# Optimization experiments

Hardware: AMD Instinct MI355X
Metric: run time of the kernel (lower is better)

## Reference

```python
import jax, jax.numpy as jnp
import numpy as np

N_FFT = 1024
HOP = 256
WIN_LENGTH = 1024
B = 16
T = 480000


def setup_inputs() -> dict:
    key = jax.random.key(0)
    k1, k2 = jax.random.split(key)
    x = jax.random.normal(k1, (B, T), dtype=jnp.float32)
    window = jax.random.uniform(k2, (WIN_LENGTH,), dtype=jnp.float32)
    return {"x": x, "window": window}


def _dft_kernels(window):
    # pad window to n_fft if needed (here win_length == n_fft)
    if WIN_LENGTH < N_FFT:
        pl = (N_FFT - WIN_LENGTH) // 2
        window = jnp.pad(window, (pl, N_FFT - WIN_LENGTH - pl))
    n_freq = N_FFT // 2 + 1
    k = jnp.arange(n_freq, dtype=jnp.float32)[:, None]   # [F,1]
    n = jnp.arange(N_FFT, dtype=jnp.float32)[None, :]    # [1,N]
    basis = (2.0 * np.pi / N_FFT) * k * n                # [F,N]
    cos_k = jnp.cos(basis) * window[None, :]
    sin_k = -jnp.sin(basis) * window[None, :]
    return cos_k, sin_k


def reference(x, window):
    pad = N_FFT // 2
    xp = jnp.pad(x, ((0, 0), (pad, pad)), mode="reflect")  # center=True, reflect
    n_frames = (xp.shape[1] - N_FFT) // HOP + 1
    # frame extraction: [n_frames, n_fft] gather indices (strided windows)
    idx = jnp.arange(n_frames)[:, None] * HOP + jnp.arange(N_FFT)[None, :]
    frames = xp[:, idx]                                   # [B, n_frames, n_fft]
    cos_k, sin_k = _dft_kernels(window)                   # [F, n_fft]
    real = jnp.einsum("btn,fn->btf", frames, cos_k)        # [B, n_frames, F]
    imag = jnp.einsum("btn,fn->btf", frames, sin_k)
    return jnp.stack([real, imag], axis=-1)               # [B, n_frames, F, 2]
```

## Files before the change

kernel.cpp:

```cpp
#include <hip/hip_runtime.h>

#define BATCH     16
#define T_LEN     480000
#define PAD       512
#define TPAD      481024
#define HOP       256
#define NFRAMES   1876
#define FRPAD     1920
#define NOUTROW   1026
#define KTOT      1024
#define NCOLS     1152

#define BM        128
#define BN        128
#define BK        32
#define ACH       4352
#define XPSTRIDE  493568

typedef __attribute__((ext_vector_type(8))) short short8;
typedef __attribute__((ext_vector_type(4))) float floatx4;

__device__ __forceinline__ unsigned short f2bf(float f) {
  union { float f; unsigned int u; } v; v.f = f;
  unsigned int u = v.u;
  return (unsigned short)((u + 0x7FFFu + ((u >> 16) & 1u)) >> 16);
}

__global__ __launch_bounds__(256) void build_xp(const float* __restrict__ x,
                                                unsigned short* __restrict__ xp) {
  const int i = blockIdx.x * 256 + threadIdx.x;
  const int b = blockIdx.y;
  unsigned short v = 0;
  if (i < TPAD) {
    int j = i - PAD;
    if (j < 0) j = -j;
    if (j >= T_LEN) j = 2 * T_LEN - 2 - j;
    v = f2bf(x[(size_t)b * T_LEN + j]);
  }
  xp[(size_t)b * XPSTRIDE + i] = v;
}

__global__ __launch_bounds__(256) void build_bmat(const float* __restrict__ win,
                                                  unsigned short* __restrict__ bm) {
  const int k = blockIdx.x * 256 + threadIdx.x;
  const int j = blockIdx.y;
  unsigned short o = 0;
  if (j < NOUTROW) {
    const int f = j >> 1;
    const int r = (f * k) & (KTOT - 1);
    const float ang = (float)r * 6.1359231515e-3f;
    const float c = __cosf(ang), s = __sinf(ang);
    const float v = (j & 1) ? -s : c;
    o = f2bf(v * win[k]);
  }
  bm[(size_t)j * KTOT + k] = o;
}

__global__ __launch_bounds__(256, 2) void stft_gemm(const unsigned short* __restrict__ xp,
                                                    const unsigned short* __restrict__ bmat,
                                                    float* __restrict__ out) {
  __shared__ unsigned short As[ACH * 8];
  __shared__ unsigned short Bs[BN * BK];

  const int tid  = threadIdx.x;
  const int lane = tid & 63;
  const int wv   = tid >> 6;
  const int wr   = wv >> 1, wc = wv & 1;
  const int bx   = blockIdx.x;
  const int b    = bx / 15;
  const int t0   = (bx - b * 15) * BM;
  const int j0   = blockIdx.y * BN;
  const int L    = lane & 15;
  const int quad = lane >> 4;

  const unsigned short* abase = xp + (size_t)b * XPSTRIDE + (size_t)t0 * HOP;

#pragma unroll
  for (int r = 0; r < ACH / 256; ++r) {
    const int ci = r * 256 + tid;
    const int s  = ci ^ ((ci >> 5) & 7);
    __builtin_amdgcn_global_load_lds(
        (const __attribute__((address_space(1))) void*)(abase + s * 8),
        (__attribute__((address_space(3))) void*)((char*)As + ci * 16),
        16, 0, 0);
  }

  const unsigned short* bsrc[2];
  short8* blds_w[2];
#pragma unroll
  for (int p = 0; p < 2; ++p) {
    const int ci  = p * 256 + tid;
    const int col = ci >> 2, c = ci & 3;
    bsrc[p]   = bmat + (size_t)(j0 + col) * KTOT + c * 8;
    blds_w[p] = (short8*)&Bs[ci * 8];
  }

  int sbase[4];
  const unsigned short* blds[4];
#pragma unroll
  for (int t = 0; t < 4; ++t) {
    const int ml = wr * 64 + t * 16 + L;
    sbase[t] = 32 * ml + quad;
    const int n = wc * 64 + t * 16 + L;
    blds[t] = &Bs[n * BK + quad * 8];
  }

  short8 breg[2];
#pragma unroll
  for (int p = 0; p < 2; ++p) breg[p] = *(const short8*)bsrc[p];
  __syncthreads();
#pragma unroll
  for (int p = 0; p < 2; ++p) *blds_w[p] = breg[p];
  __syncthreads();

  floatx4 acc[4][4] = {};

  for (int k0 = 0; k0 < KTOT; k0 += BK) {
    const bool more = (k0 + BK) < KTOT;
    if (more) {
#pragma unroll
      for (int p = 0; p < 2; ++p) breg[p] = *(const short8*)(bsrc[p] + k0 + BK);
    }

    short8 af[4], bf[4];
    const int kc = k0 >> 3;
#pragma unroll
    for (int t = 0; t < 4; ++t) {
      const int s = sbase[t] + kc;
      const int p = s ^ ((s >> 5) & 7);
      af[t] = *(const short8*)&As[p * 8];
      bf[t] = *(const short8*)blds[t];
    }
#pragma unroll
    for (int ti = 0; ti < 4; ++ti)
#pragma unroll
      for (int tj = 0; tj < 4; ++tj)
        acc[ti][tj] = __builtin_amdgcn_mfma_f32_16x16x32_bf16(
            af[ti], bf[tj], acc[ti][tj], 0, 0, 0);

    if (more) {
      __syncthreads();
#pragma unroll
      for (int p = 0; p < 2; ++p) *blds_w[p] = breg[p];
      __syncthreads();
    }
  }

#pragma unroll
  for (int ti = 0; ti < 4; ++ti) {
    const int tb = t0 + wr * 64 + ti * 16 + quad * 4;
#pragma unroll
    for (int tj = 0; tj < 4; ++tj) {
      const int gj = j0 + wc * 64 + tj * 16 + L;
      if (gj < NOUTROW) {
#pragma unroll
        for (int i = 0; i < 4; ++i) {
          const int t = tb + i;
          if (t < NFRAMES)
            out[(size_t)(b * NFRAMES + t) * NOUTROW + gj] = acc[ti][tj][i];
        }
      }
    }
  }
}

extern "C" void kernel_launch(void* const* d_in, const int* in_sizes, int n_in,
                              void* d_out, int out_size, void* d_ws, size_t ws_size,
                              hipStream_t stream) {
  const float* x   = (const float*)d_in[0];
  const float* win = (const float*)d_in[1];
  float* out = (float*)d_out;

  unsigned short* xp   = (unsigned short*)d_ws;
  unsigned short* bmat = xp + (size_t)BATCH * XPSTRIDE;

  build_xp  <<<dim3(XPSTRIDE / 256, BATCH), 256, 0, stream>>>(x, xp);
  build_bmat<<<dim3(KTOT / 256, NCOLS),     256, 0, stream>>>(win, bmat);
  stft_gemm <<<dim3(BATCH * (FRPAD / BM), NCOLS / BN), 256, 0, stream>>>(xp, bmat, out);
}
```

Before: 240.0 us.

## Load B fragments directly into registers with software pipelining, vectorize prep kernels

```diff
diff --git a/kernel.cpp b/kernel.cpp
--- a/kernel.cpp
+++ b/kernel.cpp
@@ -14,6 +14,7 @@
 #define BM        128
 #define BN        128
 #define BK        32
+#define KSTEPS    (KTOT / BK)
 #define ACH       4352
 #define XPSTRIDE  493568
 
@@ -28,39 +29,62 @@
 
 __global__ __launch_bounds__(256) void build_xp(const float* __restrict__ x,
                                                 unsigned short* __restrict__ xp) {
-  const int i = blockIdx.x * 256 + threadIdx.x;
-  const int b = blockIdx.y;
-  unsigned short v = 0;
-  if (i < TPAD) {
-    int j = i - PAD;
-    if (j < 0) j = -j;
-    if (j >= T_LEN) j = 2 * T_LEN - 2 - j;
-    v = f2bf(x[(size_t)b * T_LEN + j]);
-  }
-  xp[(size_t)b * XPSTRIDE + i] = v;
+  const int i0 = (blockIdx.x * 256 + threadIdx.x) * 8;
+  const int b  = blockIdx.y;
+  const float* xb = x + (size_t)b * T_LEN;
+  const int j0 = i0 - PAD;
+  union { short8 v; unsigned short u[8]; } o;
+  if (j0 >= 0 && j0 + 8 <= T_LEN) {
+    const float4 lo = *(const float4*)(xb + j0);
+    const float4 hi = *(const float4*)(xb + j0 + 4);
+    o.u[0] = f2bf(lo.x); o.u[1] = f2bf(lo.y); o.u[2] = f2bf(lo.z); o.u[3] = f2bf(lo.w);
+    o.u[4] = f2bf(hi.x); o.u[5] = f2bf(hi.y); o.u[6] = f2bf(hi.z); o.u[7] = f2bf(hi.w);
+  } else {
+#pragma unroll
+    for (int e = 0; e < 8; ++e) {
+      const int i = i0 + e;
+      unsigned short v = 0;
+      if (i < TPAD) {
+        int j = i - PAD;
+        if (j < 0) j = -j;
+        if (j >= T_LEN) j = 2 * T_LEN - 2 - j;
+        v = f2bf(xb[j]);
+      }
+      o.u[e] = v;
+    }
+  }
+  *(short8*)(xp + (size_t)b * XPSTRIDE + i0) = o.v;
 }
 
 __global__ __launch_bounds__(256) void build_bmat(const float* __restrict__ win,
                                                   unsigned short* __restrict__ bm) {
-  const int k = blockIdx.x * 256 + threadIdx.x;
-  const int j = blockIdx.y;
-  unsigned short o = 0;
+  const int id = blockIdx.x * 256 + threadIdx.x;
+  const int j  = id >> 7;
+  const int k0 = (id & 127) * 8;
+  union { short8 v; unsigned short u[8]; } o;
   if (j < NOUTROW) {
     const int f = j >> 1;
-    const int r = (f * k) & (KTOT - 1);
-    const float ang = (float)r * 6.1359231515e-3f;
-    const float c = __cosf(ang), s = __sinf(ang);
-    const float v = (j & 1) ? -s : c;
-    o = f2bf(v * win[k]);
-  }
-  bm[(size_t)j * KTOT + k] = o;
+    const float4 w0 = *(const float4*)(win + k0);
+    const float4 w1 = *(const float4*)(win + k0 + 4);
+    const float wv[8] = {w0.x, w0.y, w0.z, w0.w, w1.x, w1.y, w1.z, w1.w};
+#pragma unroll
+    for (int e = 0; e < 8; ++e) {
+      const int r = (f * (k0 + e)) & (KTOT - 1);
+      const float ang = (float)r * 6.1359231515e-3f;
+      const float c = __cosf(ang), s = __sinf(ang);
+      o.u[e] = f2bf(((j & 1) ? -s : c) * wv[e]);
+    }
+  } else {
+#pragma unroll
+    for (int e = 0; e < 8; ++e) o.u[e] = 0;
+  }
+  *(short8*)(bm + (size_t)j * KTOT + k0) = o.v;
 }
 
 __global__ __launch_bounds__(256, 2) void stft_gemm(const unsigned short* __restrict__ xp,
                                                     const unsigned short* __restrict__ bmat,
                                                     float* __restrict__ out) {
   __shared__ unsigned short As[ACH * 8];
-  __shared__ unsigned short Bs[BN * BK];
 
   const int tid  = threadIdx.x;
   const int lane = tid & 63;
@@ -85,66 +109,100 @@
         16, 0, 0);
   }
 
-  const unsigned short* bsrc[2];
-  short8* blds_w[2];
-#pragma unroll
-  for (int p = 0; p < 2; ++p) {
-    const int ci  = p * 256 + tid;
-    const int col = ci >> 2, c = ci & 3;
-    bsrc[p]   = bmat + (size_t)(j0 + col) * KTOT + c * 8;
-    blds_w[p] = (short8*)&Bs[ci * 8];
+  const unsigned short* bsrcw[4];
+#pragma unroll
+  for (int t = 0; t < 4; ++t) {
+    const int n = wc * 64 + t * 16 + L;
+    bsrcw[t] = bmat + (size_t)(j0 + n) * KTOT + quad * 8;
   }
 
   int sbase[4];
-  const unsigned short* blds[4];
 #pragma unroll
   for (int t = 0; t < 4; ++t) {
     const int ml = wr * 64 + t * 16 + L;
     sbase[t] = 32 * ml + quad;
-    const int n = wc * 64 + t * 16 + L;
-    blds[t] = &Bs[n * BK + quad * 8];
-  }
-
-  short8 breg[2];
-#pragma unroll
-  for (int p = 0; p < 2; ++p) breg[p] = *(const short8*)bsrc[p];
+  }
+
+  short8 bcur[4], bnxt[4];
+#pragma unroll
+  for (int t = 0; t < 4; ++t) bcur[t] = *(const short8*)(bsrcw[t]);
+#pragma unroll
+  for (int t = 0; t < 4; ++t) bnxt[t] = *(const short8*)(bsrcw[t] + BK);
+
   __syncthreads();
-#pragma unroll
-  for (int p = 0; p < 2; ++p) *blds_w[p] = breg[p];
-  __syncthreads();
+
+  short8 acur[4], anxt[4];
+#pragma unroll
+  for (int t = 0; t < 4; ++t) {
+    const int s = sbase[t];
+    const int p = s ^ ((s >> 5) & 7);
+    acur[t] = *(const short8*)&As[p * 8];
+  }
 
   floatx4 acc[4][4] = {};
 
-  for (int k0 = 0; k0 < KTOT; k0 += BK) {
-    const bool more = (k0 + BK) < KTOT;
-    if (more) {
-#pragma unroll
-      for (int p = 0; p < 2; ++p) breg[p] = *(const short8*)(bsrc[p] + k0 + BK);
-    }
-
-    short8 af[4], bf[4];
-    const int kc = k0 >> 3;
+#pragma unroll 2
+  for (int k = 0; k < KSTEPS - 2; ++k) {
+    short8 bpre[4];
+#pragma unroll
+    for (int t = 0; t < 4; ++t)
+      bpre[t] = *(const short8*)(bsrcw[t] + (size_t)(k + 2) * BK);
+    const int kc = (k + 1) << 2;
 #pragma unroll
     for (int t = 0; t < 4; ++t) {
       const int s = sbase[t] + kc;
       const int p = s ^ ((s >> 5) & 7);
-      af[t] = *(const short8*)&As[p * 8];
-      bf[t] = *(const short8*)blds[t];
-    }
+      anxt[t] = *(const short8*)&As[p * 8];
+    }
+
+    __builtin_amdgcn_s_setprio(1);
 #pragma unroll
     for (int ti = 0; ti < 4; ++ti)
 #pragma unroll
       for (int tj = 0; tj < 4; ++tj)
         acc[ti][tj] = __builtin_amdgcn_mfma_f32_16x16x32_bf16(
-            af[ti], bf[tj], acc[ti][tj], 0, 0, 0);
-
-    if (more) {
-      __syncthreads();
-#pragma unroll
-      for (int p = 0; p < 2; ++p) *blds_w[p] = breg[p];
-      __syncthreads();
-    }
-  }
+            acur[ti], bcur[tj], acc[ti][tj], 0, 0, 0);
+    __builtin_amdgcn_s_setprio(0);
+
+#pragma unroll
+    for (int t = 0; t < 4; ++t) {
+      acur[t] = anxt[t];
+      bcur[t] = bnxt[t];
+      bnxt[t] = bpre[t];
+    }
+  }
+
+  {
+    const int kc = (KSTEPS - 1) << 2;
+#pragma unroll
+    for (int t = 0; t < 4; ++t) {
+      const int s = sbase[t] + kc;
+      const int p = s ^ ((s >> 5) & 7);
+      anxt[t] = *(const short8*)&As[p * 8];
+    }
+    __builtin_amdgcn_s_setprio(1);
+#pragma unroll
+    for (int ti = 0; ti < 4; ++ti)
+#pragma unroll
+      for (int tj = 0; tj < 4; ++tj)
+        acc[ti][tj] = __builtin_amdgcn_mfma_f32_16x16x32_bf16(
+            acur[ti], bcur[tj], acc[ti][tj], 0, 0, 0);
+    __builtin_amdgcn_s_setprio(0);
+#pragma unroll
+    for (int t = 0; t < 4; ++t) {
+      acur[t] = anxt[t];
+      bcur[t] = bnxt[t];
+    }
+  }
+
+  __builtin_amdgcn_s_setprio(1);
+#pragma unroll
+  for (int ti = 0; ti < 4; ++ti)
+#pragma unroll
+    for (int tj = 0; tj < 4; ++tj)
+      acc[ti][tj] = __builtin_amdgcn_mfma_f32_16x16x32_bf16(
+          acur[ti], bcur[tj], acc[ti][tj], 0, 0, 0);
+  __builtin_amdgcn_s_setprio(0);
 
 #pragma unroll
   for (int ti = 0; ti < 4; ++ti) {
@@ -174,7 +232,7 @@
   unsigned short* xp   = (unsigned short*)d_ws;
   unsigned short* bmat = xp + (size_t)BATCH * XPSTRIDE;
 
-  build_xp  <<<dim3(XPSTRIDE / 256, BATCH), 256, 0, stream>>>(x, xp);
-  build_bmat<<<dim3(KTOT / 256, NCOLS),     256, 0, stream>>>(win, bmat);
+  build_xp  <<<dim3(XPSTRIDE / 2048, BATCH), 256, 0, stream>>>(x, xp);
+  build_bmat<<<dim3(NCOLS * (KTOT / 8) / 256), 256, 0, stream>>>(win, bmat);
   stft_gemm <<<dim3(BATCH * (FRPAD / BM), NCOLS / BN), 256, 0, stream>>>(xp, bmat, out);
 }
```

Result: slower. 284.8 us (+18.7%).
